# Optimization experiments

Hardware: AMD Instinct MI355X
Metric: run time of the kernel (lower is better)

Reference implementation:

```python
import jax, jax.numpy as jnp
import numpy as np
from jax import lax

HEADS = 4
DIM = 64
GATE_HID = 16


def setup_inputs() -> dict:
    key = jax.random.key(0)
    ks = jax.random.split(key, 12)
    b, c, h, w = 2, DIM, 48, 48
    s = 0.05
    x = jax.random.normal(ks[0], (b, c, h, w), jnp.float32)
    Wqkv = jax.random.normal(ks[1], (3 * c, c), jnp.float32) * s
    bqkv = jax.random.normal(ks[2], (3 * c,), jnp.float32) * s
    Wpos = jax.random.normal(ks[3], (3 * c, 1, 3, 3), jnp.float32) * s
    bpos = jax.random.normal(ks[4], (3 * c,), jnp.float32) * s
    Wg1 = jax.random.normal(ks[5], (GATE_HID, 1), jnp.float32) * 0.5
    bg1 = jax.random.normal(ks[6], (GATE_HID,), jnp.float32) * 0.1
    Wg2 = jax.random.normal(ks[7], (1, GATE_HID), jnp.float32) * 0.5
    bg2 = jax.random.normal(ks[8], (1,), jnp.float32) * 0.1
    Wproj = jax.random.normal(ks[9], (c, c), jnp.float32) * s
    bproj = jax.random.normal(ks[10], (c,), jnp.float32) * s
    return {"x": x, "Wqkv": Wqkv, "bqkv": bqkv, "Wpos": Wpos, "bpos": bpos,
            "Wg1": Wg1, "bg1": bg1, "Wg2": Wg2, "bg2": bg2,
            "Wproj": Wproj, "bproj": bproj}


def _forward(x, Wqkv, bqkv, Wpos, bpos, Wg1, bg1, Wg2, bg2, Wproj, bproj):
    b, c, h, w = x.shape
    n = h * w
    heads = HEADS
    hd = c // heads
    scale = hd ** -0.5
    # qkv 1x1 conv then 3x3 depthwise positional conv
    qkv = jnp.einsum('bchw,oc->bohw', x, Wqkv) + bqkv[None, :, None, None]
    qkv = lax.conv_general_dilated(
        qkv, Wpos, window_strides=(1, 1), padding='SAME',
        feature_group_count=3 * c,
        dimension_numbers=('NCHW', 'OIHW', 'NCHW')) + bpos[None, :, None, None]
    q, k, v = jnp.split(qkv, 3, axis=1)

    def to_heads(t):
        # [b,c,h,w] -> [b,heads,n,hd]
        return t.reshape(b, c, n).transpose(0, 2, 1).reshape(b, n, heads, hd).transpose(0, 2, 1, 3)

    q, k, v = to_heads(q), to_heads(k), to_heads(v)
    attn = jnp.einsum('bhid,bhjd->bhij', q, k) * scale  # [b,heads,n,n]
    prob = jax.nn.softmax(attn, axis=-1)
    entropy = -(prob * jnp.log(jnp.clip(prob, 1e-12))).sum(-1).mean(-1)  # [b,heads]
    # entropy gate: sigmoid(fc2(relu(fc1(e)))) * 0.9 + 0.1
    hgate = jax.nn.relu(entropy[..., None] @ Wg1.T + bg1)  # [b,heads,16]
    ratio = jax.nn.sigmoid(hgate @ Wg2.T + bg2)[..., 0] * 0.9 + 0.1  # [b,heads]
    # dynamic per-(batch,head) top-k along rows via rank threshold
    keep = jnp.clip(jnp.ceil(ratio * n).astype(jnp.int32), 1, n)  # [b,heads]
    sorted_desc = -jnp.sort(-attn, axis=-1)  # [b,heads,n,n]
    idx = jnp.broadcast_to((keep - 1)[:, :, None, None], (b, heads, n, 1))
    thresh = jnp.take_along_axis(sorted_desc, idx, axis=-1)  # [b,heads,n,1]
    sparse = jnp.where(attn >= thresh, attn, -jnp.inf)
    p = jax.nn.softmax(sparse, axis=-1)
    out = jnp.einsum('bhij,bhjd->bhid', p, v)  # [b,heads,n,hd]
    out = out.transpose(0, 2, 1, 3).reshape(b, n, c)
    out = out @ Wproj.T + bproj
    return out.transpose(0, 2, 1).reshape(b, c, h, w)


def reference(x, Wqkv, bqkv, Wpos, bpos, Wg1, bg1, Wg2, bg2, Wproj, bproj):
    return _forward(x, Wqkv, bqkv, Wpos, bpos, Wg1, bg1, Wg2, bg2, Wproj, bproj)
```

## Files before the change

kernel.cpp:

```cpp
#include <hip/hip_runtime.h>
#include <hip/hip_fp16.h>


typedef _Float16 half8_t __attribute__((ext_vector_type(8)));
typedef float floatx4 __attribute__((ext_vector_type(4)));

union HU { unsigned short s; _Float16 h; };
__device__ __forceinline__ _Float16 ubits_h(unsigned short u) {
  HU c; c.s = u; return c.h;
}
__device__ __forceinline__ _Float16 key_h(unsigned k) {
  unsigned short u = (k & 0x8000u) ? (unsigned short)(k & 0x7FFFu)
                                   : (unsigned short)((~k) & 0xFFFFu);
  return ubits_h(u);
}

__global__ __launch_bounds__(256) void k_qkv(const float* __restrict__ x,
                                             const float* __restrict__ W,
                                             const float* __restrict__ bias,
                                             float* __restrict__ out,
                                             float* __restrict__ ent) {
  if (blockIdx.x == 0 && threadIdx.x < 8) ent[threadIdx.x] = 0.f;
  int blk = blockIdx.x;
  int chunk = blk % 9;
  int og = (blk / 9) % 48;
  int b = blk / (9 * 48);
  int o0 = og * 4;
  int pos = chunk * 256 + threadIdx.x;
  const float* xb = x + b * 64 * 2304 + pos;
  const float* w0 = W + (o0 + 0) * 64;
  const float* w1 = W + (o0 + 1) * 64;
  const float* w2 = W + (o0 + 2) * 64;
  const float* w3 = W + (o0 + 3) * 64;
  float a0 = bias[o0 + 0], a1 = bias[o0 + 1];
  float a2 = bias[o0 + 2], a3 = bias[o0 + 3];
#pragma unroll
  for (int c = 0; c < 64; c++) {
    float xv = xb[c * 2304];
    a0 = fmaf(w0[c], xv, a0);
    a1 = fmaf(w1[c], xv, a1);
    a2 = fmaf(w2[c], xv, a2);
    a3 = fmaf(w3[c], xv, a3);
  }
  out[(b * 192 + o0 + 0) * 2304 + pos] = a0;
  out[(b * 192 + o0 + 1) * 2304 + pos] = a1;
  out[(b * 192 + o0 + 2) * 2304 + pos] = a2;
  out[(b * 192 + o0 + 3) * 2304 + pos] = a3;
}

__global__ __launch_bounds__(256) void k_dw(const float* __restrict__ qkv,
                                            const float* __restrict__ Wpos,
                                            const float* __restrict__ bpos,
                                            _Float16* __restrict__ q2,
                                            _Float16* __restrict__ k2,
                                            _Float16* __restrict__ vt) {
  __shared__ float smem[8][384];
  int blk = blockIdx.x;
  int chunk = blk % 9;
  int half = (blk / 9) % 2;
  int sel = (blk / 18) % 3;
  int head = (blk / 54) % 4;
  int b = blk / 216;
  int chbase = sel * 64 + head * 16 + half * 8;
  int bh = b * 4 + head;
  int tid = threadIdx.x;
  int p0 = chunk * 256;
  int baserow = p0 / 48;
  int rA = min(max(baserow - 1, 0), 40);

  const float* src = qkv + (size_t)(b * 192 + chbase) * 2304;
#pragma unroll
  for (int l = 0; l < 12; l++) {
    int idx = tid + l * 256;
    int ch = idx / 384;
    int off = idx - ch * 384;
    int rr = off / 48;
    int cc = off - rr * 48;
    smem[ch][off] = src[(size_t)ch * 2304 + (rA + rr) * 48 + cc];
  }
  __syncthreads();

  int pos = p0 + tid;
  int yy = pos / 48, xx = pos - yy * 48;
  int ry = yy - rA;
  float accv[8];
#pragma unroll
  for (int d = 0; d < 8; d++) {
    const float* w = Wpos + (chbase + d) * 9;
    float a = bpos[chbase + d];
#pragma unroll
    for (int dy = -1; dy <= 1; dy++) {
      int y2 = yy + dy;
      if ((unsigned)y2 < 48u) {
#pragma unroll
        for (int dx = -1; dx <= 1; dx++) {
          int x2 = xx + dx;
          if ((unsigned)x2 < 48u)
            a = fmaf(w[(dy + 1) * 3 + (dx + 1)], smem[d][(ry + dy) * 48 + x2],
                     a);
        }
      }
    }
    accv[d] = a;
  }

  if (sel == 2) {
#pragma unroll
    for (int d = 0; d < 8; d++)
      vt[((size_t)bh * 16 + half * 8 + d) * 2304 + pos] = (_Float16)accv[d];
  } else {
    _Float16 h1[8], h2[8];
#pragma unroll
    for (int d = 0; d < 8; d++) {
      float a = (sel == 0) ? accv[d] * 0.25f : accv[d];
      h1[d] = (_Float16)a;
      h2[d] = (_Float16)(a - (float)h1[d]);
    }
    _Float16* dst = ((sel == 0) ? q2 : k2) + ((size_t)bh * 2304 + pos) * 32;
    *(uint4*)(dst + half * 8) = *(uint4*)&h1[0];
    *(uint4*)(dst + 16 + half * 8) = *(uint4*)&h2[0];
  }
}

template <bool STORE>
__global__ __launch_bounds__(256) void k_ent_t(const _Float16* __restrict__ q2,
                                               const _Float16* __restrict__ k2,
                                               float* __restrict__ ent,
                                               _Float16* __restrict__ lgH) {
  __shared__ __align__(16) _Float16 tBuf[4][16][72];
  __shared__ float sWv[4][16], uWv[4][16];

  int blk = blockIdx.x;
  int rowtile = blk % 144;
  int bh = blk / 144;
  int row0 = rowtile * 16;
  int tid = threadIdx.x, lane = tid & 63, wave = tid >> 6;
  int m16 = lane & 15, quad = lane >> 4;

  const half8_t* q2v =
      (const half8_t*)(q2 + ((size_t)bh * 2304 + row0 + m16) * 32);
  half8_t A1 = q2v[quad];
  half8_t zh = {};
  half8_t A2 = (lane < 32) ? A1 : zh;
  const half8_t* kbase = (const half8_t*)(k2 + (size_t)bh * 2304 * 32);

  float s[4] = {0.f, 0.f, 0.f, 0.f}, u[4] = {0.f, 0.f, 0.f, 0.f};
  for (int g = 0; g < 9; g++) {
#pragma unroll
    for (int tt = 0; tt < 4; tt++) {
      int t = g * 4 + tt;
      int col = wave * 576 + t * 16 + m16;
      const half8_t* kk = kbase + (size_t)col * 4;
      half8_t b1 = kk[quad & 1];
      half8_t b2 = kk[2 + (quad & 1)];
      floatx4 acc = {};
      acc = __builtin_amdgcn_mfma_f32_16x16x32_f16(A2, b2, acc, 0, 0, 0);
      acc = __builtin_amdgcn_mfma_f32_16x16x32_f16(A1, b1, acc, 0, 0, 0);
#pragma unroll
      for (int i = 0; i < 4; i++) {
        if (STORE) tBuf[wave][quad * 4 + i][tt * 16 + m16] = (_Float16)acc[i];
        float e = __expf(acc[i]);
        s[i] += e;
        u[i] = fmaf(acc[i], e, u[i]);
      }
    }
    if (STORE) {
      __syncthreads();
      int rb = lane >> 3, seg = lane & 7;
#pragma unroll
      for (int it = 0; it < 2; it++) {
        int rr = it * 8 + rb;
        uint4 vv = *(const uint4*)&tBuf[wave][rr][seg * 8];
        *(uint4*)(lgH + ((size_t)bh * 2304 + row0 + rr) * 2304 + wave * 576 +
                  g * 64 + seg * 8) = vv;
      }
      __syncthreads();
    }
  }
#pragma unroll
  for (int off = 1; off < 16; off <<= 1) {
#pragma unroll
    for (int i = 0; i < 4; i++) {
      s[i] += __shfl_xor(s[i], off);
      u[i] += __shfl_xor(u[i], off);
    }
  }
  if (m16 == 0) {
#pragma unroll
    for (int i = 0; i < 4; i++) {
      sWv[wave][quad * 4 + i] = s[i];
      uWv[wave][quad * 4 + i] = u[i];
    }
  }
  __syncthreads();
  if (tid < 16) {
    float S = sWv[0][tid] + sWv[1][tid] + sWv[2][tid] + sWv[3][tid];
    float U = uWv[0][tid] + uWv[1][tid] + uWv[2][tid] + uWv[3][tid];
    float er = __logf(S) - U / S;
    er += __shfl_xor(er, 1);
    er += __shfl_xor(er, 2);
    er += __shfl_xor(er, 4);
    er += __shfl_xor(er, 8);
    if (tid == 0) atomicAdd(&ent[bh], er);
  }
}

#define EXPPACK8H(B, IT)                                           \
  {                                                                \
    float p0 = (hv[B + 0] >= th_h) ? __expf((float)hv[B + 0]) : 0.f; \
    float p1 = (hv[B + 1] >= th_h) ? __expf((float)hv[B + 1]) : 0.f; \
    float p2 = (hv[B + 2] >= th_h) ? __expf((float)hv[B + 2]) : 0.f; \
    float p3 = (hv[B + 3] >= th_h) ? __expf((float)hv[B + 3]) : 0.f; \
    float p4 = (hv[B + 4] >= th_h) ? __expf((float)hv[B + 4]) : 0.f; \
    float p5 = (hv[B + 5] >= th_h) ? __expf((float)hv[B + 5]) : 0.f; \
    float p6 = (hv[B + 6] >= th_h) ? __expf((float)hv[B + 6]) : 0.f; \
    float p7 = (hv[B + 7] >= th_h) ? __expf((float)hv[B + 7]) : 0.f; \
    sp += ((p0 + p1) + (p2 + p3)) + ((p4 + p5) + (p6 + p7));       \
    uint4 o;                                                       \
    __half2 h0 = __floats2half2_rn(p0, p1); o.x = *(unsigned*)&h0; \
    __half2 h1 = __floats2half2_rn(p2, p3); o.y = *(unsigned*)&h1; \
    __half2 h2 = __floats2half2_rn(p4, p5); o.z = *(unsigned*)&h2; \
    __half2 h3 = __floats2half2_rn(p6, p7); o.w = *(unsigned*)&h3; \
    prow4[lane + IT * 64] = o;                                     \
  }

template <bool CACHED>
__global__ __launch_bounds__(256, 7) void k_attn_t(
    const _Float16* __restrict__ q2, const _Float16* __restrict__ k2,
    const _Float16* __restrict__ vt, const _Float16* __restrict__ lgH,
    const float* __restrict__ ent, const float* __restrict__ Wg1,
    const float* __restrict__ bg1, const float* __restrict__ Wg2,
    const float* __restrict__ bg2, float* __restrict__ oh) {
  __shared__ __align__(16) _Float16 pbuf[4][2320];
  __shared__ float sS[4];
  __shared__ __align__(16) float redSh[4][64];

  int a = blockIdx.x;
  int v8 = a & 7;
  int idx = a >> 3;
  int q = idx & 3;
  int pi = idx >> 2;
  int bh = pi / 18;
  int rowtile = v8 + (pi % 18) * 8;
  int rowblk = rowtile * 4 + q;
  int row0 = rowblk * 4;
  int tid = threadIdx.x, lane = tid & 63, wave = tid >> 6;

  float eAvg = ent[bh] * (1.f / 2304.f);
  float gacc = bg2[0];
#pragma unroll
  for (int i = 0; i < 16; i++) {
    float h = fmaxf(fmaf(eAvg, Wg1[i], bg1[i]), 0.f);
    gacc = fmaf(h, Wg2[i], gacc);
  }
  float ratio = 0.9f / (1.f + __expf(-gacc)) + 0.1f;
  int kp = (int)ceilf(ratio * 2304.f);
  unsigned keep = (unsigned)min(max(kp, 1), 2304);

  unsigned wb[18];
  if (CACHED) {
    const _Float16* src = lgH + ((size_t)bh * 2304 + row0 + wave) * 2304;
    const uint4* s4 = (const uint4*)src;
    uint4 r0 = s4[lane];
    uint4 r1 = s4[lane + 64];
    uint4 r2 = s4[lane + 128];
    uint4 r3 = s4[lane + 192];
    uint2 r4 = *(const uint2*)(src + 2048 + lane * 4);
    wb[0] = r0.x; wb[1] = r0.y; wb[2] = r0.z; wb[3] = r0.w;
    wb[4] = r1.x; wb[5] = r1.y; wb[6] = r1.z; wb[7] = r1.w;
    wb[8] = r2.x; wb[9] = r2.y; wb[10] = r2.z; wb[11] = r2.w;
    wb[12] = r3.x; wb[13] = r3.y; wb[14] = r3.z; wb[15] = r3.w;
    wb[16] = r4.x; wb[17] = r4.y;
  } else {
    int m16 = lane & 15, quad = lane >> 4;
    const half8_t* q2v =
        (const half8_t*)(q2 + ((size_t)bh * 2304 + row0 + (m16 & 3)) * 32);
    half8_t A1 = q2v[quad];
    half8_t zh = {};
    half8_t A2 = (lane < 32) ? A1 : zh;
    const half8_t* kbase = (const half8_t*)(k2 + (size_t)bh * 2304 * 32);
#pragma unroll 4
    for (int t = 0; t < 36; t++) {
      int ct = wave * 36 + t;
      int col = ct * 16 + m16;
      const half8_t* kk = kbase + (size_t)col * 4;
      half8_t b1 = kk[quad & 1];
      half8_t b2 = kk[2 + (quad & 1)];
      floatx4 acc = {};
      acc = __builtin_amdgcn_mfma_f32_16x16x32_f16(A2, b2, acc, 0, 0, 0);
      acc = __builtin_amdgcn_mfma_f32_16x16x32_f16(A1, b1, acc, 0, 0, 0);
      if (lane < 16) {
#pragma unroll
        for (int i = 0; i < 4; i++) pbuf[i][ct * 16 + lane] = (_Float16)acc[i];
      }
    }
    __syncthreads();
    const _Float16* src = pbuf[wave];
    const uint4* s4 = (const uint4*)src;
    uint4 r0 = s4[lane];
    uint4 r1 = s4[lane + 64];
    uint4 r2 = s4[lane + 128];
    uint4 r3 = s4[lane + 192];
    uint2 r4 = *(const uint2*)(src + 2048 + lane * 4);
    wb[0] = r0.x; wb[1] = r0.y; wb[2] = r0.z; wb[3] = r0.w;
    wb[4] = r1.x; wb[5] = r1.y; wb[6] = r1.z; wb[7] = r1.w;
    wb[8] = r2.x; wb[9] = r2.y; wb[10] = r2.z; wb[11] = r2.w;
    wb[12] = r3.x; wb[13] = r3.y; wb[14] = r3.z; wb[15] = r3.w;
    wb[16] = r4.x; wb[17] = r4.y;
  }

  _Float16 hv[36];
#pragma unroll
  for (int i = 0; i < 18; i++) {
    hv[2 * i + 0] = ubits_h((unsigned short)(wb[i] & 0xFFFFu));
    hv[2 * i + 1] = ubits_h((unsigned short)(wb[i] >> 16));
  }
#pragma unroll
  for (int i = 0; i < 36; i++) asm("" : "+v"(hv[i]));

  _Float16 th_h;
  {
    unsigned T = 0u;
    for (int bit = 15; bit >= 0; --bit) {
      unsigned cand = T | (1u << bit);
      _Float16 cth = key_h(cand);
      unsigned cnt = 0u;
#pragma unroll
      for (int i = 0; i < 36; i++)
        cnt += (unsigned)__popcll(__ballot(hv[i] >= cth));
      if (cnt >= keep) {
        T = cand;
        if (cnt == keep) break;
      }
    }
    th_h = key_h(T);
  }

  {
    float sp = 0.f;
    uint4* prow4 = (uint4*)pbuf[wave];
    EXPPACK8H(0, 0);
    EXPPACK8H(8, 1);
    EXPPACK8H(16, 2);
    EXPPACK8H(24, 3);
    {
      float p0 = (hv[32] >= th_h) ? __expf((float)hv[32]) : 0.f;
      float p1 = (hv[33] >= th_h) ? __expf((float)hv[33]) : 0.f;
      float p2 = (hv[34] >= th_h) ? __expf((float)hv[34]) : 0.f;
      float p3 = (hv[35] >= th_h) ? __expf((float)hv[35]) : 0.f;
      sp += (p0 + p1) + (p2 + p3);
      uint2 o;
      __half2 h0 = __floats2half2_rn(p0, p1); o.x = *(unsigned*)&h0;
      __half2 h1 = __floats2half2_rn(p2, p3); o.y = *(unsigned*)&h1;
      *(uint2*)(pbuf[wave] + 2048 + lane * 4) = o;
    }
#pragma unroll
    for (int off = 1; off < 64; off <<= 1) sp += __shfl_xor(sp, off);
    if (lane == 0) sS[wave] = sp;
  }
  __syncthreads();

  {
    int m16 = lane & 15, quad = lane >> 4;
    const _Float16* vrow = vt + ((size_t)bh * 16 + m16) * 2304;
    const _Float16* prow = pbuf[m16 & 3];
    int jb0 = wave * 576 + quad * 8;
    floatx4 acc = {};
#pragma unroll 6
    for (int t = 0; t < 18; t++) {
      int jb = jb0 + t * 32;
      half8_t a2 = *(const half8_t*)&prow[jb];
      half8_t b2 = *(const half8_t*)&vrow[jb];
      acc = __builtin_amdgcn_mfma_f32_16x16x32_f16(a2, b2, acc, 0, 0, 0);
    }
    if (lane < 16) {
      *(floatx4*)&redSh[wave][m16 * 4] = acc;
    }
  }
  __syncthreads();
  if (tid < 64) {
    int r = tid & 3, d = tid >> 2;
    float s2 = redSh[0][d * 4 + r] + redSh[1][d * 4 + r] +
               redSh[2][d * 4 + r] + redSh[3][d * 4 + r];
    oh[((size_t)(bh * 2304 + row0 + r)) * 16 + d] = s2 / sS[r];
  }
}

__global__ __launch_bounds__(256) void k_proj(const float* __restrict__ oh,
                                              const float* __restrict__ Wp,
                                              const float* __restrict__ bp,
                                              float* __restrict__ out) {
  int blk = blockIdx.x;
  int chunk = blk % 9;
  int cog = (blk / 9) % 16;
  int b = blk / (9 * 16);
  int co0 = cog * 4;
  int pos = chunk * 256 + threadIdx.x;
  float a0 = bp[co0 + 0], a1 = bp[co0 + 1], a2 = bp[co0 + 2], a3 = bp[co0 + 3];
#pragma unroll
  for (int head = 0; head < 4; head++) {
    const float4* op =
        (const float4*)(oh + ((size_t)((b * 4 + head) * 2304 + pos)) * 16);
#pragma unroll
    for (int p = 0; p < 4; p++) {
      float4 o4 = op[p];
#pragma unroll
      for (int i = 0; i < 4; i++) {
        const float* wr = Wp + (co0 + i) * 64 + head * 16 + p * 4;
        float* ai = (i == 0) ? &a0 : ((i == 1) ? &a1 : ((i == 2) ? &a2 : &a3));
        *ai = fmaf(wr[0], o4.x, *ai);
        *ai = fmaf(wr[1], o4.y, *ai);
        *ai = fmaf(wr[2], o4.z, *ai);
        *ai = fmaf(wr[3], o4.w, *ai);
      }
    }
  }
  out[(b * 64 + co0 + 0) * 2304 + pos] = a0;
  out[(b * 64 + co0 + 1) * 2304 + pos] = a1;
  out[(b * 64 + co0 + 2) * 2304 + pos] = a2;
  out[(b * 64 + co0 + 3) * 2304 + pos] = a3;
}

extern "C" void kernel_launch(void* const* d_in, const int* in_sizes, int n_in,
                              void* d_out, int out_size, void* d_ws,
                              size_t ws_size, hipStream_t stream) {
  const float* x    = (const float*)d_in[0];
  const float* Wqkv = (const float*)d_in[1];
  const float* bqkv = (const float*)d_in[2];
  const float* Wpos = (const float*)d_in[3];
  const float* bpos = (const float*)d_in[4];
  const float* Wg1  = (const float*)d_in[5];
  const float* bg1  = (const float*)d_in[6];
  const float* Wg2  = (const float*)d_in[7];
  const float* bg2  = (const float*)d_in[8];
  const float* Wpr  = (const float*)d_in[9];
  const float* bpr  = (const float*)d_in[10];
  float* out = (float*)d_out;

  const size_t lgBytes = (size_t)8 * 2304 * 2304 * 2;
  const size_t baseBytes = (size_t)(884736 + 294912 + 8) * 4 +
                           (size_t)(2 * 589824 + 294912) * 2;
  bool cached = ws_size >= lgBytes + baseBytes;

  char* base = (char*)d_ws;
  _Float16* lgH = nullptr;
  if (cached) {
    lgH = (_Float16*)base;
    base += lgBytes;
  }
  float* qkv_raw = (float*)base;
  float* oh = qkv_raw + 884736;
  float* ent = oh + 294912;
  _Float16* q2 = (_Float16*)(ent + 8);
  _Float16* k2 = q2 + 589824;
  _Float16* vt = k2 + 589824;

  hipLaunchKernelGGL(k_qkv, dim3(2 * 48 * 9), dim3(256), 0, stream,
                     x, Wqkv, bqkv, qkv_raw, ent);
  hipLaunchKernelGGL(k_dw, dim3(432), dim3(256), 0, stream,
                     qkv_raw, Wpos, bpos, q2, k2, vt);
  if (cached) {
    hipLaunchKernelGGL((k_ent_t<true>), dim3(8 * 144), dim3(256), 0, stream,
                       q2, k2, ent, lgH);
    hipLaunchKernelGGL((k_attn_t<true>), dim3(8 * 576), dim3(256), 0, stream,
                       q2, k2, vt, lgH, ent, Wg1, bg1, Wg2, bg2, oh);
  } else {
    hipLaunchKernelGGL((k_ent_t<false>), dim3(8 * 144), dim3(256), 0, stream,
                       q2, k2, ent, lgH);
    hipLaunchKernelGGL((k_attn_t<false>), dim3(8 * 576), dim3(256), 0, stream,
                       q2, k2, vt, lgH, ent, Wg1, bg1, Wg2, bg2, oh);
  }
  hipLaunchKernelGGL(k_proj, dim3(2 * 16 * 9), dim3(256), 0, stream,
                     oh, Wpr, bpr, out);
}
```

Before: 196.8 us.

## Replace bitwise ballot radix search with two-pass LDS histogram top-k threshold select

The per-row k-th largest threshold was found by a 16-step bit-by-bit search, each step doing 36 ballots and popcounts. It is now found with a two-pass 8-bit radix select: LDS atomic histograms over order-preserving keys, then a wave prefix scan to pick the bucket. This cuts the selection work to two histogram passes, at the cost of LDS atomics that can contend when many values share a bucket. Occupancy in the launch bounds also drops from 7 to 6 blocks to leave room for the extra key registers.

```diff
diff --git a/kernel.cpp b/kernel.cpp
--- a/kernel.cpp
+++ b/kernel.cpp
@@ -13,6 +13,34 @@
   unsigned short u = (k & 0x8000u) ? (unsigned short)(k & 0x7FFFu)
                                    : (unsigned short)((~k) & 0xFFFFu);
   return ubits_h(u);
+}
+
+__device__ __forceinline__ uint2 hist_select(const unsigned* hist, int lane,
+                                             unsigned keepN) {
+  uint4 cc = ((const uint4*)hist)[lane];
+  unsigned inc = cc.x + cc.y + cc.z + cc.w;
+#pragma unroll
+  for (int off = 1; off < 64; off <<= 1) {
+    unsigned t = __shfl_up(inc, off);
+    if (lane >= off) inc += t;
+  }
+  unsigned total = __shfl(inc, 63);
+  unsigned above = total - inc;
+  unsigned a3 = above;
+  unsigned a2 = a3 + cc.w;
+  unsigned a1 = a2 + cc.z;
+  unsigned a0 = a1 + cc.y;
+  bool has = false;
+  unsigned B_l = 0, A_l = 0;
+  if (a3 < keepN && a3 + cc.w >= keepN) { has = true; B_l = lane * 4 + 3; A_l = a3; }
+  else if (a2 < keepN && a2 + cc.z >= keepN) { has = true; B_l = lane * 4 + 2; A_l = a2; }
+  else if (a1 < keepN && a1 + cc.y >= keepN) { has = true; B_l = lane * 4 + 1; A_l = a1; }
+  else if (a0 < keepN && a0 + cc.x >= keepN) { has = true; B_l = lane * 4 + 0; A_l = a0; }
+  unsigned long long m = __ballot(has);
+  int src = __ffsll(m) - 1;
+  unsigned B = __shfl(B_l, src);
+  unsigned run = __shfl(A_l, src);
+  return make_uint2(B, run);
 }
 
 __global__ __launch_bounds__(256) void k_qkv(const float* __restrict__ x,
@@ -205,27 +233,35 @@
   }
 }
 
-#define EXPPACK8H(B, IT)                                           \
-  {                                                                \
-    float p0 = (hv[B + 0] >= th_h) ? __expf((float)hv[B + 0]) : 0.f; \
-    float p1 = (hv[B + 1] >= th_h) ? __expf((float)hv[B + 1]) : 0.f; \
-    float p2 = (hv[B + 2] >= th_h) ? __expf((float)hv[B + 2]) : 0.f; \
-    float p3 = (hv[B + 3] >= th_h) ? __expf((float)hv[B + 3]) : 0.f; \
-    float p4 = (hv[B + 4] >= th_h) ? __expf((float)hv[B + 4]) : 0.f; \
-    float p5 = (hv[B + 5] >= th_h) ? __expf((float)hv[B + 5]) : 0.f; \
-    float p6 = (hv[B + 6] >= th_h) ? __expf((float)hv[B + 6]) : 0.f; \
-    float p7 = (hv[B + 7] >= th_h) ? __expf((float)hv[B + 7]) : 0.f; \
-    sp += ((p0 + p1) + (p2 + p3)) + ((p4 + p5) + (p6 + p7));       \
-    uint4 o;                                                       \
-    __half2 h0 = __floats2half2_rn(p0, p1); o.x = *(unsigned*)&h0; \
-    __half2 h1 = __floats2half2_rn(p2, p3); o.y = *(unsigned*)&h1; \
-    __half2 h2 = __floats2half2_rn(p4, p5); o.z = *(unsigned*)&h2; \
-    __half2 h3 = __floats2half2_rn(p6, p7); o.w = *(unsigned*)&h3; \
-    prow4[lane + IT * 64] = o;                                     \
+#define EXPPACKW(W0, IT)                                              \
+  {                                                                   \
+    _Float16 h0 = ubits_h((unsigned short)(wb[W0 + 0] & 0xFFFFu));    \
+    _Float16 h1 = ubits_h((unsigned short)(wb[W0 + 0] >> 16));        \
+    _Float16 h2 = ubits_h((unsigned short)(wb[W0 + 1] & 0xFFFFu));    \
+    _Float16 h3 = ubits_h((unsigned short)(wb[W0 + 1] >> 16));        \
+    _Float16 h4 = ubits_h((unsigned short)(wb[W0 + 2] & 0xFFFFu));    \
+    _Float16 h5 = ubits_h((unsigned short)(wb[W0 + 2] >> 16));        \
+    _Float16 h6 = ubits_h((unsigned short)(wb[W0 + 3] & 0xFFFFu));    \
+    _Float16 h7 = ubits_h((unsigned short)(wb[W0 + 3] >> 16));        \
+    float p0 = (h0 >= th_h) ? __expf((float)h0) : 0.f;                \
+    float p1 = (h1 >= th_h) ? __expf((float)h1) : 0.f;                \
+    float p2 = (h2 >= th_h) ? __expf((float)h2) : 0.f;                \
+    float p3 = (h3 >= th_h) ? __expf((float)h3) : 0.f;                \
+    float p4 = (h4 >= th_h) ? __expf((float)h4) : 0.f;                \
+    float p5 = (h5 >= th_h) ? __expf((float)h5) : 0.f;                \
+    float p6 = (h6 >= th_h) ? __expf((float)h6) : 0.f;                \
+    float p7 = (h7 >= th_h) ? __expf((float)h7) : 0.f;                \
+    sp += ((p0 + p1) + (p2 + p3)) + ((p4 + p5) + (p6 + p7));          \
+    uint4 o;                                                          \
+    __half2 q0 = __floats2half2_rn(p0, p1); o.x = *(unsigned*)&q0;    \
+    __half2 q1 = __floats2half2_rn(p2, p3); o.y = *(unsigned*)&q1;    \
+    __half2 q2h = __floats2half2_rn(p4, p5); o.z = *(unsigned*)&q2h;  \
+    __half2 q3 = __floats2half2_rn(p6, p7); o.w = *(unsigned*)&q3;    \
+    prow4[lane + IT * 64] = o;                                        \
   }
 
 template <bool CACHED>
-__global__ __launch_bounds__(256, 7) void k_attn_t(
+__global__ __launch_bounds__(256, 6) void k_attn_t(
     const _Float16* __restrict__ q2, const _Float16* __restrict__ k2,
     const _Float16* __restrict__ vt, const _Float16* __restrict__ lgH,
     const float* __restrict__ ent, const float* __restrict__ Wg1,
@@ -309,49 +345,59 @@
     wb[16] = r4.x; wb[17] = r4.y;
   }
 
-  _Float16 hv[36];
-#pragma unroll
-  for (int i = 0; i < 18; i++) {
-    hv[2 * i + 0] = ubits_h((unsigned short)(wb[i] & 0xFFFFu));
-    hv[2 * i + 1] = ubits_h((unsigned short)(wb[i] >> 16));
-  }
-#pragma unroll
-  for (int i = 0; i < 36; i++) asm("" : "+v"(hv[i]));
-
   _Float16 th_h;
   {
-    unsigned T = 0u;
-    for (int bit = 15; bit >= 0; --bit) {
-      unsigned cand = T | (1u << bit);
-      _Float16 cth = key_h(cand);
-      unsigned cnt = 0u;
-#pragma unroll
-      for (int i = 0; i < 36; i++)
-        cnt += (unsigned)__popcll(__ballot(hv[i] >= cth));
-      if (cnt >= keep) {
-        T = cand;
-        if (cnt == keep) break;
-      }
-    }
-    th_h = key_h(T);
+    unsigned* hist = (unsigned*)&pbuf[wave][0];
+    unsigned kb[18];
+#pragma unroll
+    for (int i = 0; i < 18; i++)
+      kb[i] = wb[i] ^ (((wb[i] >> 15) & 0x00010001u) * 0x7FFFu + 0x80008000u);
+
+#pragma unroll
+    for (int i = 0; i < 4; i++) hist[lane + i * 64] = 0u;
+#pragma unroll
+    for (int i = 0; i < 18; i++) {
+      atomicAdd(&hist[(kb[i] >> 8) & 0xFFu], 1u);
+      atomicAdd(&hist[kb[i] >> 24], 1u);
+    }
+    uint2 s1 = hist_select(hist, lane, keep);
+    unsigned B = s1.x;
+    unsigned keep2 = keep - s1.y;
+
+#pragma unroll
+    for (int i = 0; i < 4; i++) hist[lane + i * 64] = 0u;
+#pragma unroll
+    for (int i = 0; i < 18; i++) {
+      unsigned klo = kb[i] & 0xFFFFu;
+      unsigned khi = kb[i] >> 16;
+      if ((klo >> 8) == B) atomicAdd(&hist[klo & 0xFFu], 1u);
+      if ((khi >> 8) == B) atomicAdd(&hist[khi & 0xFFu], 1u);
+    }
+    uint2 s2 = hist_select(hist, lane, keep2);
+    unsigned K = (B << 8) | s2.x;
+    th_h = key_h(K);
   }
 
   {
     float sp = 0.f;
     uint4* prow4 = (uint4*)pbuf[wave];
-    EXPPACK8H(0, 0);
-    EXPPACK8H(8, 1);
-    EXPPACK8H(16, 2);
-    EXPPACK8H(24, 3);
+    EXPPACKW(0, 0);
+    EXPPACKW(4, 1);
+    EXPPACKW(8, 2);
+    EXPPACKW(12, 3);
     {
-      float p0 = (hv[32] >= th_h) ? __expf((float)hv[32]) : 0.f;
-      float p1 = (hv[33] >= th_h) ? __expf((float)hv[33]) : 0.f;
-      float p2 = (hv[34] >= th_h) ? __expf((float)hv[34]) : 0.f;
-      float p3 = (hv[35] >= th_h) ? __expf((float)hv[35]) : 0.f;
+      _Float16 h0 = ubits_h((unsigned short)(wb[16] & 0xFFFFu));
+      _Float16 h1 = ubits_h((unsigned short)(wb[16] >> 16));
+      _Float16 h2 = ubits_h((unsigned short)(wb[17] & 0xFFFFu));
+      _Float16 h3 = ubits_h((unsigned short)(wb[17] >> 16));
+      float p0 = (h0 >= th_h) ? __expf((float)h0) : 0.f;
+      float p1 = (h1 >= th_h) ? __expf((float)h1) : 0.f;
+      float p2 = (h2 >= th_h) ? __expf((float)h2) : 0.f;
+      float p3 = (h3 >= th_h) ? __expf((float)h3) : 0.f;
       sp += (p0 + p1) + (p2 + p3);
       uint2 o;
-      __half2 h0 = __floats2half2_rn(p0, p1); o.x = *(unsigned*)&h0;
-      __half2 h1 = __floats2half2_rn(p2, p3); o.y = *(unsigned*)&h1;
+      __half2 q0 = __floats2half2_rn(p0, p1); o.x = *(unsigned*)&q0;
+      __half2 q1 = __floats2half2_rn(p2, p3); o.y = *(unsigned*)&q1;
       *(uint2*)(pbuf[wave] + 2048 + lane * 4) = o;
     }
 #pragma unroll
```

After: 194.0 us. About the same (-1.4%).
